# Kernel tuning notes

Hardware: AMD Instinct MI355X
Metric: run time of the kernel (lower is better)

Reference implementation:

```python
import jax, jax.numpy as jnp
import numpy as np

N0, N1, N2 = 200000, 50000, 10000   # node counts per hop (src -> layer1 targets -> layer2 targets)
E1, E2 = 1000000, 250000
C_IN, H = 128, 256


def setup_inputs() -> dict:
    key = jax.random.key(0)
    ks = jax.random.split(key, 10)
    return {
        "x": jax.random.normal(ks[0], (N0, C_IN), dtype=jnp.float32),
        "src1": jax.random.randint(ks[1], (E1,), 0, N0, dtype=jnp.int32),
        "dst1": jax.random.randint(ks[2], (E1,), 0, N1, dtype=jnp.int32),
        "src2": jax.random.randint(ks[3], (E2,), 0, N1, dtype=jnp.int32),
        "dst2": jax.random.randint(ks[4], (E2,), 0, N2, dtype=jnp.int32),
        "Wl1": jax.random.normal(ks[5], (C_IN, H), dtype=jnp.float32) / np.sqrt(C_IN),
        "Wr1": jax.random.normal(ks[6], (C_IN, H), dtype=jnp.float32) / np.sqrt(C_IN),
        "b1": jnp.zeros((H,), dtype=jnp.float32),
        "Wl2": jax.random.normal(ks[7], (H, H), dtype=jnp.float32) / np.sqrt(H),
        "Wr2": jax.random.normal(ks[8], (H, H), dtype=jnp.float32) / np.sqrt(H),
        "b2": jnp.zeros((H,), dtype=jnp.float32),
    }


def _sage_conv(x_src, x_dst, src, dst, Wl, Wr, b, n_dst):
    # mean aggregation of neighbor messages (PyG SAGEConv, aggr='mean', root_weight=True)
    msgs = x_src[src]                                             # [E, C] irregular gather
    agg = jax.ops.segment_sum(msgs, dst, num_segments=n_dst)      # [n_dst, C]
    cnt = jax.ops.segment_sum(jnp.ones_like(dst, dtype=x_src.dtype), dst, num_segments=n_dst)
    agg = agg / jnp.maximum(cnt, 1.0)[:, None]
    return agg @ Wl + x_dst @ Wr + b


def reference(x, src1, dst1, src2, dst2, Wl1, Wr1, b1, Wl2, Wr2, b2):
    # layer 1: targets are first N1 nodes
    h = _sage_conv(x, x[:N1], src1, dst1, Wl1, Wr1, b1, N1)       # [N1, H]
    h = jax.nn.relu(h)                                            # dropout: eval mode (identity)
    # layer 2: targets are first N2 nodes of the layer-1 output
    out = _sage_conv(h, h[:N2], src2, dst2, Wl2, Wr2, b2, N2)     # [N2, H]
    return out
```

## Files before the change

kernel.cpp:

```cpp
#include <hip/hip_runtime.h>

#define N0 200000
#define N1 50000
#define N2 10000
#define E1 1000000
#define E2 250000
#define CIN 128
#define HD  256

#define SH1   6
#define PK1   18
#define NB1   782
#define CAP1  2048
#define DPB1  64
#define SH2   4
#define PK2   16
#define NB2   625
#define CAP2  640
#define DPB2  16

#define NBIN1 489
#define NBIN2 123
#define NPREP 768
#define NCVT  25000

#define EB1   (CAP1 + 512)
#define EB2   (CAP2 + 128)

typedef __attribute__((ext_vector_type(8))) short short8;
typedef __attribute__((ext_vector_type(4))) float f32x4;
typedef __attribute__((ext_vector_type(2))) float f32x2;

__device__ __forceinline__ unsigned short f2bf(float f) {
    unsigned u = __builtin_bit_cast(unsigned, f);
    u = (u + 0x7fffu + ((u >> 16) & 1u)) >> 16;
    return (unsigned short)u;
}
__device__ __forceinline__ float bf2f(unsigned short h) {
    unsigned u = ((unsigned)h) << 16;
    return __builtin_bit_cast(float, u);
}

__device__ __forceinline__ unsigned enc_fp8x4(float a, float b, float c, float d) {
#if __has_builtin(__builtin_amdgcn_cvt_pk_fp8_f32)
    int p = 0;
    p = __builtin_amdgcn_cvt_pk_fp8_f32(a, b, p, false);
    p = __builtin_amdgcn_cvt_pk_fp8_f32(c, d, p, true);
    return (unsigned)p;
#else
    float vv[4] = {a, b, c, d};
    unsigned out = 0;
    #pragma unroll
    for (int k = 0; k < 4; k++) {
        float f = fminf(fmaxf(vv[k], -448.f), 448.f);
        unsigned u = __builtin_bit_cast(unsigned, f);
        const unsigned s = (u >> 24) & 0x80u;
        u &= 0x7fffffffu;
        unsigned byte;
        if (u < 0x3C800000u) {
            const float af = __builtin_bit_cast(float, u);
            byte = s | (unsigned)(int)rintf(af * 512.0f);
        } else {
            const unsigned u2 = u + 0x000FFFFFu + ((u >> 20) & 1u);
            const unsigned e  = (u2 >> 23) - 120u;
            byte = s | ((e & 0xFu) << 3) | ((u2 >> 20) & 7u);
        }
        out |= byte << (8 * k);
    }
    return out;
#endif
}

__device__ __forceinline__ unsigned char enc_fp8_1(float v) {
#if __has_builtin(__builtin_amdgcn_cvt_pk_fp8_f32)
    const int p = __builtin_amdgcn_cvt_pk_fp8_f32(v, v, 0, false);
    return (unsigned char)(p & 0xFF);
#else
    float f = fminf(fmaxf(v, -448.f), 448.f);
    unsigned u = __builtin_bit_cast(unsigned, f);
    const unsigned s = (u >> 24) & 0x80u;
    u &= 0x7fffffffu;
    unsigned byte;
    if (u < 0x3C800000u) {
        const float af = __builtin_bit_cast(float, u);
        byte = s | (unsigned)(int)rintf(af * 512.0f);
    } else {
        const unsigned u2 = u + 0x000FFFFFu + ((u >> 20) & 1u);
        const unsigned e  = (u2 >> 23) - 120u;
        byte = s | ((e & 0xFu) << 3) | ((u2 >> 20) & 7u);
    }
    return (unsigned char)byte;
#endif
}

__device__ __forceinline__ void acc_fp8x4(unsigned w, float* __restrict__ acc) {
#if __has_builtin(__builtin_amdgcn_cvt_pk_f32_fp8)
    const f32x2 lo = __builtin_amdgcn_cvt_pk_f32_fp8((int)w, false);
    const f32x2 hi = __builtin_amdgcn_cvt_pk_f32_fp8((int)w, true);
    acc[0] += lo[0]; acc[1] += lo[1]; acc[2] += hi[0]; acc[3] += hi[1];
#else
    #pragma unroll
    for (int k = 0; k < 4; k++) {
        const unsigned b8   = (w >> (8 * k)) & 0xFFu;
        const unsigned bits = ((b8 & 0x80u) << 24) | ((b8 & 0x7Fu) << 20);
        acc[k] += __builtin_bit_cast(float, bits) * 0x1p120f;
    }
#endif
}

template<int SHIFTB, int PACKSH, int CAP>
__device__ __forceinline__ void bin_body(
    int bb, const int* __restrict__ src, const int* __restrict__ dst,
    int* __restrict__ gcnt, unsigned* __restrict__ binned, int E, int* sh)
{
    int* hcnt  = sh;
    int* hbase = sh + 1024;
    int* hcur  = sh + 2048;
    const int t = threadIdx.x;
    #pragma unroll
    for (int j = 0; j < 4; j++) hcnt[t + j * 256] = 0;
    __syncthreads();

    unsigned pk[8];
    int      bk[8];
    const int e0 = bb * 2048;
    #pragma unroll
    for (int j = 0; j < 8; j++) {
        const int e = e0 + j * 256 + t;
        if (e < E) {
            const int d = dst[e];
            const int s = src[e];
            bk[j] = d >> SHIFTB;
            pk[j] = ((unsigned)(d & ((1 << SHIFTB) - 1)) << PACKSH) | (unsigned)s;
            atomicAdd(&hcnt[bk[j]], 1);
        } else bk[j] = -1;
    }
    __syncthreads();

    #pragma unroll
    for (int j = 0; j < 4; j++) {
        const int i = t + j * 256;
        hbase[i] = atomicAdd(&gcnt[i], hcnt[i]);
        hcur[i]  = 0;
    }
    __syncthreads();

    #pragma unroll
    for (int j = 0; j < 8; j++) {
        if (bk[j] >= 0) {
            const int idx = atomicAdd(&hcur[bk[j]], 1);
            binned[(size_t)bk[j] * CAP + hbase[bk[j]] + idx] = pk[j];
        }
    }
}

__global__ __launch_bounds__(256) void megaA_kernel(
    const float* __restrict__ x, unsigned short* __restrict__ xb,
    unsigned char* __restrict__ xf8, unsigned char* __restrict__ hb8,
    const float* __restrict__ Wl1, const float* __restrict__ Wr1,
    const float* __restrict__ Wl2, const float* __restrict__ Wr2,
    unsigned short* __restrict__ wsw1, unsigned short* __restrict__ wsw2,
    const int* __restrict__ src1, const int* __restrict__ dst1,
    const int* __restrict__ src2, const int* __restrict__ dst2,
    int* __restrict__ gcnt1, int* __restrict__ gcnt2,
    unsigned* __restrict__ binned1, unsigned* __restrict__ binned2)
{
    __shared__ int sh[3072];
    const int b = blockIdx.x;
    const int t = threadIdx.x;

    if (b < NBIN1) {
        bin_body<SH1, PK1, CAP1>(b, src1, dst1, gcnt1, binned1, E1, sh);
    } else if (b < NBIN1 + NBIN2) {
        bin_body<SH2, PK2, CAP2>(b - NBIN1, src2, dst2, gcnt2, binned2, E2, sh);
    } else if (b < NBIN1 + NBIN2 + NPREP) {
        const int pb = b - NBIN1 - NBIN2;
        const float* Wl; const float* Wr; unsigned short* wsw; int K, tid;
        if (pb < 256) { Wl = Wl1; Wr = Wr1; wsw = wsw1; K = CIN; tid = pb * 256 + t; }
        else          { Wl = Wl2; Wr = Wr2; wsw = wsw2; K = HD;  tid = (pb - 256) * 256 + t; }
        const int j  = tid & 7;
        const int L  = (tid >> 3) & 63;
        const int nt = (tid >> 9) & 15;
        const int kt = tid >> 13;
        const int k  = kt * 32 + (L >> 4) * 8 + j;
        const int n  = nt * 16 + (L & 15);
        const float v = (k < K) ? Wl[(size_t)k * HD + n]
                                : Wr[(size_t)(k - K) * HD + n];
        wsw[tid] = f2bf(v);
    } else if (b < NBIN1 + NBIN2 + NPREP + NCVT) {
        const int i = (b - NBIN1 - NBIN2 - NPREP) * 256 + t;
        const f32x4 v = __builtin_nontemporal_load(&((const f32x4*)x)[i]);
        ((unsigned*)xf8)[i] = enc_fp8x4(v.x, v.y, v.z, v.w);
        if (i < N1 * (CIN / 4)) {
            ushort4 o;
            o.x = f2bf(v.x); o.y = f2bf(v.y); o.z = f2bf(v.z); o.w = f2bf(v.w);
            ((ushort4*)xb)[i] = o;
        }
    } else {
        if (t < 32)  ((unsigned*)(xf8 + (size_t)N0 * CIN))[t] = 0u;
        if (t < 64)  ((unsigned*)(hb8 + (size_t)N1 * HD))[t] = 0u;
    }
}

__global__ __launch_bounds__(512) void layer1_mega(
    const unsigned short* __restrict__ xb, const unsigned char* __restrict__ xf8,
    const unsigned* __restrict__ binned1, const int* __restrict__ gcnt1,
    const unsigned short* __restrict__ wsw1, const float* __restrict__ bias,
    unsigned short* __restrict__ hb, unsigned char* __restrict__ hb8)
{
    __shared__ int ebuf[EB1];
    __shared__ int lhist[DPB1], loff[DPB1], lcur[DPB1];
    __shared__ __align__(16) unsigned short aggT[4 * DPB1 * 4 * 8];

    const int t = threadIdx.x;
    const int b = blockIdx.x;
    const int cnt = gcnt1[b];
    const unsigned* bp = binned1 + (size_t)b * CAP1;

    if (t < DPB1) lhist[t] = 0;
    __syncthreads();
    for (int i = t; i < cnt; i += 512)
        atomicAdd(&lhist[bp[i] >> PK1], 1);
    __syncthreads();
    if (t < DPB1) {
        const int p8 = (lhist[t] + 7) & ~7;
        int sum = p8;
        #pragma unroll
        for (int ofs = 1; ofs < DPB1; ofs <<= 1) {
            const int u = __shfl_up(sum, ofs);
            if (t >= ofs) sum += u;
        }
        const int st = sum - p8;
        loff[t] = st; lcur[t] = st;
    }
    __syncthreads();
    for (int i = t; i < cnt; i += 512) {
        const unsigned p = bp[i];
        const int slot = atomicAdd(&lcur[p >> PK1], 1);
        ebuf[slot] = (int)(p & ((1u << PK1) - 1u));
    }
    __syncthreads();
    if (t < DPB1) {
        const int h = lhist[t];
        const int np = (h + 7) & ~7;
        const int s0 = loff[t];
        for (int i = s0 + h; i < s0 + np; i++) ebuf[i] = N0;
    }
    __syncthreads();

    const int w = t >> 6, L = t & 63;
    const int qd = L >> 4, l16 = L & 15;
    const unsigned char* xp8 = xf8 + (size_t)l16 * 8;
    #pragma unroll 1
    for (int rr = 0; rr < 2; rr++) {
        const int r = w * 8 + rr * 4 + qd;
        const int base = loff[r];
        const int n    = lhist[r];
        const int npad = (n + 7) & ~7;
        float acc[8];
        #pragma unroll
        for (int j = 0; j < 8; j++) acc[j] = 0.f;
        for (int i = 0; i < npad; i += 8) {
            uint2 v[8];
            #pragma unroll
            for (int u = 0; u < 8; u++) {
                const int s = ebuf[base + i + u];
                v[u] = *(const uint2*)(xp8 + (size_t)s * CIN);
            }
            #pragma unroll
            for (int u = 0; u < 8; u++) {
                acc_fp8x4(v[u].x, acc);
                acc_fp8x4(v[u].y, acc + 4);
            }
        }
        const float sc = 1.0f / fmaxf((float)n, 1.0f);
        short8 o;
        #pragma unroll
        for (int j = 0; j < 8; j++) o[j] = (short)f2bf(acc[j] * sc);
        const int kt = l16 >> 2, q = l16 & 3;
        *(short8*)&aggT[((kt * DPB1 + r) * 4 + q) * 8] = o;
    }
    __syncthreads();

    const int m = L & 15, q = L >> 4;
    const int mt = w & 3, nh = w >> 2;
    const int row_l = mt * 16 + m;
    const int rg2 = min(b * DPB1 + row_l, N1 - 1);
    const unsigned short* a2p = xb + (size_t)rg2 * CIN + q * 8;

    f32x4 acc[8];
    #pragma unroll
    for (int nt = 0; nt < 8; nt++) acc[nt] = (f32x4){0.f, 0.f, 0.f, 0.f};

    #pragma unroll
    for (int kt = 0; kt < 8; kt++) {
        short8 af;
        if (kt < 4) af = *(const short8*)&aggT[((kt * DPB1 + row_l) * 4 + q) * 8];
        else        af = *(const short8*)(a2p + (kt - 4) * 32);
        #pragma unroll
        for (int nt = 0; nt < 8; nt++) {
            const short8 bf = *(const short8*)(
                wsw1 + (((size_t)kt * 16 + (nh * 8 + nt)) * 64 + L) * 8);
            acc[nt] = __builtin_amdgcn_mfma_f32_16x16x32_bf16(af, bf, acc[nt], 0, 0, 0);
        }
    }

    const int orow0 = b * DPB1 + mt * 16 + q * 4;
    #pragma unroll
    for (int nt = 0; nt < 8; nt++) {
        const int col = (nh * 8 + nt) * 16 + m;
        const float bv = bias[col];
        #pragma unroll
        for (int r = 0; r < 4; r++) {
            const int row = orow0 + r;
            if (row < N1) {
                const float v = fmaxf(acc[nt][r] + bv, 0.0f);
                hb8[(size_t)row * HD + col] = enc_fp8_1(v);
                if (row < N2) hb[(size_t)row * HD + col] = f2bf(v);
            }
        }
    }
}

__global__ __launch_bounds__(512) void layer2_mega(
    const unsigned short* __restrict__ hb, const unsigned char* __restrict__ hb8,
    const unsigned* __restrict__ binned2, const int* __restrict__ gcnt2,
    const unsigned short* __restrict__ wsw2, const float* __restrict__ bias,
    float* __restrict__ outp)
{
    __shared__ int ebuf[EB2];
    __shared__ int lhist[DPB2], loff[DPB2], lcur[DPB2];
    __shared__ __align__(16) unsigned short aggT[8 * DPB2 * 4 * 8];

    const int t = threadIdx.x;
    const int b = blockIdx.x;
    const int cnt = gcnt2[b];
    const unsigned* bp = binned2 + (size_t)b * CAP2;

    if (t < DPB2) lhist[t] = 0;
    __syncthreads();
    for (int i = t; i < cnt; i += 512)
        atomicAdd(&lhist[bp[i] >> PK2], 1);
    __syncthreads();
    if (t < DPB2) {
        const int p8 = (lhist[t] + 7) & ~7;
        int sum = p8;
        #pragma unroll
        for (int ofs = 1; ofs < DPB2; ofs <<= 1) {
            const int u = __shfl_up(sum, ofs);
            if (t >= ofs) sum += u;
        }
        const int st = sum - p8;
        loff[t] = st; lcur[t] = st;
    }
    __syncthreads();
    for (int i = t; i < cnt; i += 512) {
        const unsigned p = bp[i];
        const int slot = atomicAdd(&lcur[p >> PK2], 1);
        ebuf[slot] = (int)(p & 0xFFFFu);
    }
    __syncthreads();
    if (t < DPB2) {
        const int h = lhist[t];
        const int np = (h + 7) & ~7;
        const int s0 = loff[t];
        for (int i = s0 + h; i < s0 + np; i++) ebuf[i] = N1;
    }
    __syncthreads();

    const int w = t >> 6, L = t & 63;
    const int hf = L >> 5, l32 = L & 31;
    {
        const int r = w * 2 + hf;
        const int base = loff[r];
        const int n    = lhist[r];
        const int npad = (n + 7) & ~7;
        float acc[8];
        #pragma unroll
        for (int j = 0; j < 8; j++) acc[j] = 0.f;
        const unsigned char* hp8 = hb8 + (size_t)l32 * 8;
        for (int i = 0; i < npad; i += 8) {
            uint2 v[8];
            #pragma unroll
            for (int u = 0; u < 8; u++) {
                const int s = ebuf[base + i + u];
                v[u] = *(const uint2*)(hp8 + (size_t)s * HD);
            }
            #pragma unroll
            for (int u = 0; u < 8; u++) {
                acc_fp8x4(v[u].x, acc);
                acc_fp8x4(v[u].y, acc + 4);
            }
        }
        const float sc = 1.0f / fmaxf((float)n, 1.0f);
        short8 o;
        #pragma unroll
        for (int j = 0; j < 8; j++) o[j] = (short)f2bf(acc[j] * sc);
        const int kt = l32 >> 2, q = l32 & 3;
        *(short8*)&aggT[((kt * DPB2 + r) * 4 + q) * 8] = o;
    }
    __syncthreads();

    const int m = L & 15, q = L >> 4;
    const int rg2 = b * DPB2 + m;
    const unsigned short* a2p = hb + (size_t)rg2 * HD + q * 8;

    f32x4 acc[2];
    acc[0] = (f32x4){0.f, 0.f, 0.f, 0.f};
    acc[1] = (f32x4){0.f, 0.f, 0.f, 0.f};

    #pragma unroll
    for (int kt = 0; kt < 16; kt++) {
        short8 af;
        if (kt < 8) af = *(const short8*)&aggT[((kt * DPB2 + m) * 4 + q) * 8];
        else        af = *(const short8*)(a2p + (kt - 8) * 32);
        #pragma unroll
        for (int nt = 0; nt < 2; nt++) {
            const short8 bf = *(const short8*)(
                wsw2 + (((size_t)kt * 16 + (w * 2 + nt)) * 64 + L) * 8);
            acc[nt] = __builtin_amdgcn_mfma_f32_16x16x32_bf16(af, bf, acc[nt], 0, 0, 0);
        }
    }

    const int orow0 = b * DPB2 + q * 4;
    #pragma unroll
    for (int nt = 0; nt < 2; nt++) {
        const int col = (w * 2 + nt) * 16 + m;
        const float bv = bias[col];
        #pragma unroll
        for (int r = 0; r < 4; r++)
            outp[(size_t)(orow0 + r) * HD + col] = acc[nt][r] + bv;
    }
}

extern "C" void kernel_launch(void* const* d_in, const int* in_sizes, int n_in,
                              void* d_out, int out_size, void* d_ws, size_t ws_size,
                              hipStream_t stream)
{
    const float* x    = (const float*)d_in[0];
    const int*   src1 = (const int*)  d_in[1];
    const int*   dst1 = (const int*)  d_in[2];
    const int*   src2 = (const int*)  d_in[3];
    const int*   dst2 = (const int*)  d_in[4];
    const float* Wl1  = (const float*)d_in[5];
    const float* Wr1  = (const float*)d_in[6];
    const float* b1   = (const float*)d_in[7];
    const float* Wl2  = (const float*)d_in[8];
    const float* Wr2  = (const float*)d_in[9];
    const float* b2   = (const float*)d_in[10];
    float* out = (float*)d_out;

    unsigned short* xb   = (unsigned short*)d_ws;
    unsigned char*  xf8  = (unsigned char*)(xb + (size_t)N1 * CIN);
    unsigned short* hb   = (unsigned short*)(xf8 + (size_t)(N0 + 2) * CIN);
    unsigned char*  hb8  = (unsigned char*)(hb + (size_t)N2 * HD);
    unsigned short* wsw1 = (unsigned short*)(hb8 + (size_t)(N1 + 1) * HD + 256);
    unsigned short* wsw2 = wsw1 + 2 * CIN * HD;
    int* gcnt1 = (int*)(wsw2 + 2 * HD * HD);
    int* gcnt2 = gcnt1 + 1024;
    unsigned* binned1 = (unsigned*)(gcnt2 + 1024);
    unsigned* binned2 = binned1 + (size_t)NB1 * CAP1;

    hipMemsetAsync(gcnt1, 0, 2048 * sizeof(int), stream);

    megaA_kernel<<<NBIN1 + NBIN2 + NPREP + NCVT + 1, 256, 0, stream>>>(
        x, xb, xf8, hb8, Wl1, Wr1, Wl2, Wr2, wsw1, wsw2,
        src1, dst1, src2, dst2, gcnt1, gcnt2, binned1, binned2);

    layer1_mega<<<NB1, 512, 0, stream>>>(xb, xf8, binned1, gcnt1, wsw1, b1, hb, hb8);
    layer2_mega<<<NB2, 512, 0, stream>>>(hb, hb8, binned2, gcnt2, wsw2, b2, out);
}
```

Before: 267.0 us.

## Split each layer-1 bin across two blocks of 32 destination rows

Layer-1 blocks now each handle half of a 64-row bin: every block reads the full bin's edge list but keeps only edges whose destination falls in its half. Each warp aggregates one row instead of two, and the GEMM tile shrinks to 32 rows with each warp covering 4 output tiles. This doubles the grid and halves per-block shared memory, aiming for more parallelism and occupancy. The cost is that each bin's edge list is read and filtered twice and weight fragments are loaded by twice as many blocks.

```diff
diff --git a/kernel.cpp b/kernel.cpp
--- a/kernel.cpp
+++ b/kernel.cpp
@@ -13,6 +13,9 @@
 #define NB1   782
 #define CAP1  2048
 #define DPB1  64
+#define DPB1H 32
+#define NB1L  1564
+#define EB1H  1440
 #define SH2   4
 #define PK2   16
 #define NB2   625
@@ -24,7 +27,6 @@
 #define NPREP 768
 #define NCVT  25000
 
-#define EB1   (CAP1 + 512)
 #define EB2   (CAP2 + 128)
 
 typedef __attribute__((ext_vector_type(8))) short short8;
@@ -208,25 +210,29 @@
     const unsigned short* __restrict__ wsw1, const float* __restrict__ bias,
     unsigned short* __restrict__ hb, unsigned char* __restrict__ hb8)
 {
-    __shared__ int ebuf[EB1];
-    __shared__ int lhist[DPB1], loff[DPB1], lcur[DPB1];
-    __shared__ __align__(16) unsigned short aggT[4 * DPB1 * 4 * 8];
+    __shared__ int ebuf[EB1H];
+    __shared__ int lhist[DPB1H], loff[DPB1H], lcur[DPB1H];
+    __shared__ __align__(16) unsigned short aggT[4 * DPB1H * 4 * 8];
 
     const int t = threadIdx.x;
     const int b = blockIdx.x;
-    const int cnt = gcnt1[b];
-    const unsigned* bp = binned1 + (size_t)b * CAP1;
-
-    if (t < DPB1) lhist[t] = 0;
-    __syncthreads();
-    for (int i = t; i < cnt; i += 512)
-        atomicAdd(&lhist[bp[i] >> PK1], 1);
-    __syncthreads();
-    if (t < DPB1) {
+    const int B = b >> 1;
+    const int H = b & 1;
+    const int cnt = gcnt1[B];
+    const unsigned* bp = binned1 + (size_t)B * CAP1;
+
+    if (t < DPB1H) lhist[t] = 0;
+    __syncthreads();
+    for (int i = t; i < cnt; i += 512) {
+        const int r = (int)(bp[i] >> PK1) - H * DPB1H;
+        if ((unsigned)r < (unsigned)DPB1H) atomicAdd(&lhist[r], 1);
+    }
+    __syncthreads();
+    if (t < DPB1H) {
         const int p8 = (lhist[t] + 7) & ~7;
         int sum = p8;
         #pragma unroll
-        for (int ofs = 1; ofs < DPB1; ofs <<= 1) {
+        for (int ofs = 1; ofs < DPB1H; ofs <<= 1) {
             const int u = __shfl_up(sum, ofs);
             if (t >= ofs) sum += u;
         }
@@ -236,11 +242,14 @@
     __syncthreads();
     for (int i = t; i < cnt; i += 512) {
         const unsigned p = bp[i];
-        const int slot = atomicAdd(&lcur[p >> PK1], 1);
-        ebuf[slot] = (int)(p & ((1u << PK1) - 1u));
-    }
-    __syncthreads();
-    if (t < DPB1) {
+        const int r = (int)(p >> PK1) - H * DPB1H;
+        if ((unsigned)r < (unsigned)DPB1H) {
+            const int slot = atomicAdd(&lcur[r], 1);
+            ebuf[slot] = (int)(p & ((1u << PK1) - 1u));
+        }
+    }
+    __syncthreads();
+    if (t < DPB1H) {
         const int h = lhist[t];
         const int np = (h + 7) & ~7;
         const int s0 = loff[t];
@@ -251,9 +260,8 @@
     const int w = t >> 6, L = t & 63;
     const int qd = L >> 4, l16 = L & 15;
     const unsigned char* xp8 = xf8 + (size_t)l16 * 8;
-    #pragma unroll 1
-    for (int rr = 0; rr < 2; rr++) {
-        const int r = w * 8 + rr * 4 + qd;
+    {
+        const int r = w * 4 + qd;
         const int base = loff[r];
         const int n    = lhist[r];
         const int npad = (n + 7) & ~7;
@@ -278,37 +286,38 @@
         #pragma unroll
         for (int j = 0; j < 8; j++) o[j] = (short)f2bf(acc[j] * sc);
         const int kt = l16 >> 2, q = l16 & 3;
-        *(short8*)&aggT[((kt * DPB1 + r) * 4 + q) * 8] = o;
+        *(short8*)&aggT[((kt * DPB1H + r) * 4 + q) * 8] = o;
     }
     __syncthreads();
 
     const int m = L & 15, q = L >> 4;
-    const int mt = w & 3, nh = w >> 2;
+    const int mt = w & 1, nq = w >> 1;
     const int row_l = mt * 16 + m;
-    const int rg2 = min(b * DPB1 + row_l, N1 - 1);
+    const int rg2 = min(b * DPB1H + row_l, N1 - 1);
     const unsigned short* a2p = xb + (size_t)rg2 * CIN + q * 8;
 
-    f32x4 acc[8];
-    #pragma unroll
-    for (int nt = 0; nt < 8; nt++) acc[nt] = (f32x4){0.f, 0.f, 0.f, 0.f};
+    f32x4 acc[4];
+    #pragma unroll
+    for (int nt = 0; nt < 4; nt++) acc[nt] = (f32x4){0.f, 0.f, 0.f, 0.f};
 
     #pragma unroll
     for (int kt = 0; kt < 8; kt++) {
         short8 af;
-        if (kt < 4) af = *(const short8*)&aggT[((kt * DPB1 + row_l) * 4 + q) * 8];
+        if (kt < 4) af = *(const short8*)&aggT[((kt * DPB1H + row_l) * 4 + q) * 8];
         else        af = *(const short8*)(a2p + (kt - 4) * 32);
         #pragma unroll
-        for (int nt = 0; nt < 8; nt++) {
+        for (int nt = 0; nt < 4; nt++) {
+            const int ntg = nq * 4 + nt;
             const short8 bf = *(const short8*)(
-                wsw1 + (((size_t)kt * 16 + (nh * 8 + nt)) * 64 + L) * 8);
+                wsw1 + (((size_t)kt * 16 + ntg) * 64 + L) * 8);
             acc[nt] = __builtin_amdgcn_mfma_f32_16x16x32_bf16(af, bf, acc[nt], 0, 0, 0);
         }
     }
 
-    const int orow0 = b * DPB1 + mt * 16 + q * 4;
-    #pragma unroll
-    for (int nt = 0; nt < 8; nt++) {
-        const int col = (nh * 8 + nt) * 16 + m;
+    const int orow0 = b * DPB1H + mt * 16 + q * 4;
+    #pragma unroll
+    for (int nt = 0; nt < 4; nt++) {
+        const int col = (nq * 4 + nt) * 16 + m;
         const float bv = bias[col];
         #pragma unroll
         for (int r = 0; r < 4; r++) {
@@ -467,6 +476,6 @@
         x, xb, xf8, hb8, Wl1, Wr1, Wl2, Wr2, wsw1, wsw2,
         src1, dst1, src2, dst2, gcnt1, gcnt2, binned1, binned2);
 
-    layer1_mega<<<NB1, 512, 0, stream>>>(xb, xf8, binned1, gcnt1, wsw1, b1, hb, hb8);
+    layer1_mega<<<NB1L, 512, 0, stream>>>(xb, xf8, binned1, gcnt1, wsw1, b1, hb, hb8);
     layer2_mega<<<NB2, 512, 0, stream>>>(hb, hb8, binned2, gcnt2, wsw2, b2, out);
 }
```

Measured after the change: 259.1 us, median of 2. -3.0%, faster.
